# Optimization experiments

Measured on AMD Instinct MI355X. Metric: run time of the kernel, lower is better.

Reference implementation:

```python
import jax, jax.numpy as jnp
import numpy as np

B, S, D = 4, 2048, 1024  # batch, seq_len, isize; FFN hidden = isize, gate dim = 2*isize


def setup_inputs() -> dict:
    key = jax.random.key(0)
    ks = jax.random.split(key, 6)
    sc = lambda n: 1.0 / np.sqrt(n)
    return {
        "iQ": jax.random.normal(ks[0], (B, S, D), jnp.float32),
        "iV": jax.random.normal(ks[1], (B, S, D), jnp.float32),
        "W1": jax.random.normal(ks[2], (D, D), jnp.float32) * sc(D),
        "b1": jnp.zeros((D,), jnp.float32),
        "W2": jax.random.normal(ks[3], (D, D), jnp.float32) * sc(D),
        "b2": jnp.zeros((D,), jnp.float32),
        "Wg": jax.random.normal(ks[4], (2 * D, 2 * D), jnp.float32) * sc(2 * D),
        "bg": jnp.zeros((2 * D,), jnp.float32),
    }


def reference(iQ, iV, W1, b1, W2, b2, Wg, bg):
    seql = iV.shape[1]
    # AAN cumulative-average matrix: row i has 1/(i+1) in cols 0..i (lower triangular)
    inv = 1.0 / jnp.arange(1, seql + 1, dtype=iV.dtype)  # [S]
    attn = jnp.tril(jnp.broadcast_to(inv[:, None], (seql, seql)))  # [S, S]
    avg = jnp.einsum('st,btd->bsd', attn, iV)  # [B, S, D]
    # PositionwiseFF with norm_input=False, dropout=0: Linear -> ReLU -> Linear
    h = jax.nn.relu(avg @ W1 + b1)
    ffn = h @ W2 + b2  # [B, S, D]
    # sigmoid gate over concat(iQ, ffn)
    g = jax.nn.sigmoid(jnp.concatenate([iQ, ffn], axis=-1) @ Wg + bg)  # [B, S, 2D]
    d = ffn.shape[-1]
    igate = g[..., :d]
    fgate = g[..., d:]
    return igate * iQ + fgate * ffn
```

## Files before the change

### kernel.cpp

```cpp
#include <hip/hip_runtime.h>
#include <hip/hip_bf16.h>
#include <cstdint>

typedef unsigned short u16;
typedef unsigned int   u32;

typedef __attribute__((ext_vector_type(8))) short short8;
typedef __attribute__((ext_vector_type(4))) float f32x4;

__device__ __forceinline__ float b2f(u16 v) { return __uint_as_float(((u32)v) << 16); }
__device__ __forceinline__ u16 f2b(float f) {
    u32 u = __float_as_uint(f);
    u += 0x7FFFu + ((u >> 16) & 1u);
    return (u16)(u >> 16);
}

#define G2L16(gp, lp) __builtin_amdgcn_global_load_lds(                       \
    (const __attribute__((address_space(1))) void*)(gp),                      \
    (__attribute__((address_space(3))) void*)(lp), 16, 0, 0)

__device__ __forceinline__ void transpose_body(const float* __restrict__ in,
                                               u16* __restrict__ out,
                                               int R, int C, int lb, int tilesX,
                                               float (*tile)[33]) {
    const int bx = (lb % tilesX) * 32;
    const int by = (lb / tilesX) * 32;
    const int tx = threadIdx.x & 31, ty = threadIdx.x >> 5;
    #pragma unroll
    for (int i = 0; i < 32; i += 8)
        tile[ty + i][tx] = in[(size_t)(by + ty + i) * C + (bx + tx)];
    __syncthreads();
    #pragma unroll
    for (int i = 0; i < 32; i += 8)
        out[(size_t)(bx + ty + i) * R + (by + tx)] = f2b(tile[tx][ty + i]);
}

__global__ void prologue_kernel(const float* __restrict__ W1, u16* __restrict__ W1t,
                                const float* __restrict__ W2, u16* __restrict__ W2t,
                                const float* __restrict__ Wg, u16* __restrict__ Wgt,
                                const float* __restrict__ iQ, u16* __restrict__ iQb,
                                const float* __restrict__ iV, float* __restrict__ csum) {
    __shared__ float tile[32][33];
    const int bid = blockIdx.x;
    const int tid = threadIdx.x;
    if (bid < 1024) {
        transpose_body(W1, W1t, 1024, 1024, bid, 32, tile);
    } else if (bid < 2048) {
        transpose_body(W2, W2t, 1024, 1024, bid - 1024, 32, tile);
    } else if (bid < 6144) {
        transpose_body(Wg, Wgt, 2048, 2048, bid - 2048, 64, tile);
    } else if (bid < 14336) {
        const size_t i = ((size_t)(bid - 6144) * 256 + tid) * 4;
        const float4 v = *(const float4*)(iQ + i);
        ushort4 o;
        o.x = f2b(v.x); o.y = f2b(v.y); o.z = f2b(v.z); o.w = f2b(v.w);
        *(ushort4*)(iQb + i) = o;
    } else {
        const int idx = bid - 14336;
        const int b = idx >> 6, c = idx & 63;
        const int d = tid * 4;
        const float* src = iV + ((size_t)(b * 2048 + c * 32)) * 1024 + d;
        float4 s = {0.f, 0.f, 0.f, 0.f};
        #pragma unroll 8
        for (int i = 0; i < 32; ++i) {
            const float4 v = *(const float4*)(src + (size_t)i * 1024);
            s.x += v.x; s.y += v.y; s.z += v.z; s.w += v.w;
        }
        *(float4*)(csum + ((size_t)(b * 64 + c)) * 1024 + d) = s;
    }
}

__global__ void scan_kernel(const float* __restrict__ iV, const float* __restrict__ csum,
                            u16* __restrict__ avg) {
    const int c = blockIdx.x & 63, b = blockIdx.x >> 6;
    const int d = threadIdx.x * 4;
    const float* cs = csum + (size_t)b * 64 * 1024 + d;
    float4 a0 = {0,0,0,0}, a1 = {0,0,0,0}, a2 = {0,0,0,0}, a3 = {0,0,0,0};
    int cc = 0;
    for (; cc + 4 <= c; cc += 4) {
        const float4 v0 = *(const float4*)(cs + (size_t)(cc + 0) * 1024);
        const float4 v1 = *(const float4*)(cs + (size_t)(cc + 1) * 1024);
        const float4 v2 = *(const float4*)(cs + (size_t)(cc + 2) * 1024);
        const float4 v3 = *(const float4*)(cs + (size_t)(cc + 3) * 1024);
        a0.x += v0.x; a0.y += v0.y; a0.z += v0.z; a0.w += v0.w;
        a1.x += v1.x; a1.y += v1.y; a1.z += v1.z; a1.w += v1.w;
        a2.x += v2.x; a2.y += v2.y; a2.z += v2.z; a2.w += v2.w;
        a3.x += v3.x; a3.y += v3.y; a3.z += v3.z; a3.w += v3.w;
    }
    for (; cc < c; ++cc) {
        const float4 v = *(const float4*)(cs + (size_t)cc * 1024);
        a0.x += v.x; a0.y += v.y; a0.z += v.z; a0.w += v.w;
    }
    float4 acc;
    acc.x = (a0.x + a1.x) + (a2.x + a3.x);
    acc.y = (a0.y + a1.y) + (a2.y + a3.y);
    acc.z = (a0.z + a1.z) + (a2.z + a3.z);
    acc.w = (a0.w + a1.w) + (a2.w + a3.w);

    const size_t off = ((size_t)(b * 2048 + c * 32)) * 1024 + d;
    const float* src = iV + off;
    u16*         dst = avg + off;
    const int s0 = c * 32;
    #pragma unroll 4
    for (int i = 0; i < 32; ++i) {
        const float4 v = *(const float4*)(src + (size_t)i * 1024);
        acc.x += v.x; acc.y += v.y; acc.z += v.z; acc.w += v.w;
        const float inv = 1.0f / (float)(s0 + i + 1);
        ushort4 o;
        o.x = f2b(acc.x * inv); o.y = f2b(acc.y * inv);
        o.z = f2b(acc.z * inv); o.w = f2b(acc.w * inv);
        *(ushort4*)(dst + (size_t)i * 1024) = o;
    }
}

template <int EPI>
__global__ __launch_bounds__(256, 2)
void gemm_kernel(const u16* __restrict__ A, const u16* __restrict__ Bt,
                 const float* __restrict__ bias, u16* __restrict__ C,
                 int M, int N, int K) {
    __shared__ u16 As[128 * 64];
    __shared__ u16 Bs[128 * 64];

    const int tid  = threadIdx.x;
    const int m0   = blockIdx.x * 128;
    const int n0   = blockIdx.y * 128;
    const int wave = tid >> 6, lane = tid & 63;
    const int wm   = (wave & 1) << 6;
    const int wn   = (wave >> 1) << 6;
    const int quad = lane >> 4, l16 = lane & 15;

    f32x4 acc[4][4];
    #pragma unroll
    for (int i = 0; i < 4; ++i)
        #pragma unroll
        for (int j = 0; j < 4; ++j) acc[i][j] = (f32x4){0.f, 0.f, 0.f, 0.f};

    int oo[4], rr[4], qq[4];
    #pragma unroll
    for (int j = 0; j < 4; ++j) {
        oo[j] = tid * 16 + j * 4096;
        rr[j] = oo[j] >> 7;
        qq[j] = ((oo[j] >> 4) & 7) ^ (rr[j] & 7);
    }

    const int ktiles = K >> 6;
    for (int kt = 0; kt < ktiles; ++kt) {
        const int kb = kt << 6;
        #pragma unroll
        for (int j = 0; j < 4; ++j) {
            G2L16((const char*)A  + ((size_t)(m0 + rr[j]) * K + kb) * 2 + qq[j] * 16,
                  (char*)As + oo[j]);
            G2L16((const char*)Bt + ((size_t)(n0 + rr[j]) * K + kb) * 2 + qq[j] * 16,
                  (char*)Bs + oo[j]);
        }
        __syncthreads();

        #pragma unroll
        for (int h = 0; h < 2; ++h) {
            short8 af[4], bf[4];
            #pragma unroll
            for (int mi = 0; mi < 4; ++mi) {
                const int R = wm + mi * 16 + l16;
                af[mi] = *(const short8*)(As + R * 64 + ((((h << 2) | quad) ^ (R & 7)) << 3));
            }
            #pragma unroll
            for (int ni = 0; ni < 4; ++ni) {
                const int R = wn + ni * 16 + l16;
                bf[ni] = *(const short8*)(Bs + R * 64 + ((((h << 2) | quad) ^ (R & 7)) << 3));
            }
            #pragma unroll
            for (int mi = 0; mi < 4; ++mi)
                #pragma unroll
                for (int ni = 0; ni < 4; ++ni)
                    acc[mi][ni] = __builtin_amdgcn_mfma_f32_16x16x32_bf16(
                        af[mi], bf[ni], acc[mi][ni], 0, 0, 0);
        }
        __syncthreads();
    }

    #pragma unroll
    for (int ni = 0; ni < 4; ++ni) {
        const int col = n0 + wn + ni * 16 + l16;
        const float bv = bias[col];
        #pragma unroll
        for (int mi = 0; mi < 4; ++mi) {
            const int row0 = m0 + wm + mi * 16 + quad * 4;
            #pragma unroll
            for (int r = 0; r < 4; ++r) {
                float v = acc[mi][ni][r] + bv;
                if (EPI == 0) v = fmaxf(v, 0.f);
                C[(size_t)(row0 + r) * N + col] = f2b(v);
            }
        }
    }
}

__global__ __launch_bounds__(256, 2)
void gemm_gate_kernel(const u16* __restrict__ iQb, const u16* __restrict__ ffn,
                      const u16* __restrict__ Wgt, const float* __restrict__ bg,
                      const float* __restrict__ iQ, float* __restrict__ out,
                      int M, int D2 ) {
    __shared__ u16 As [128 * 64];
    __shared__ u16 Bs0[128 * 64];
    __shared__ u16 Bs1[128 * 64];

    const int tid  = threadIdx.x;
    const int m0   = blockIdx.x * 128;
    const int n0   = blockIdx.y * 128;
    const int wave = tid >> 6, lane = tid & 63;
    const int wm   = (wave & 1) << 6;
    const int wn   = (wave >> 1) << 6;
    const int quad = lane >> 4, l16 = lane & 15;
    const int D = D2 >> 1;

    f32x4 acc[2][4][4];
    #pragma unroll
    for (int p = 0; p < 2; ++p)
        #pragma unroll
        for (int i = 0; i < 4; ++i)
            #pragma unroll
            for (int j = 0; j < 4; ++j) acc[p][i][j] = (f32x4){0.f, 0.f, 0.f, 0.f};

    int oo[4], rr[4], qq[4];
    #pragma unroll
    for (int j = 0; j < 4; ++j) {
        oo[j] = tid * 16 + j * 4096;
        rr[j] = oo[j] >> 7;
        qq[j] = ((oo[j] >> 4) & 7) ^ (rr[j] & 7);
    }

    const int ktiles = D2 >> 6;
    for (int kt = 0; kt < ktiles; ++kt) {
        const int kb = kt << 6;
        const char* Ab = (const char*)((kb < D) ? (iQb + kb) : (ffn + (kb - D)));
        const char* B0 = (const char*)(Wgt + (size_t)n0 * D2 + kb);
        const char* B1 = (const char*)(Wgt + (size_t)(n0 + D) * D2 + kb);
        #pragma unroll
        for (int j = 0; j < 4; ++j) {
            G2L16(Ab + (size_t)(m0 + rr[j]) * D * 2 + qq[j] * 16, (char*)As  + oo[j]);
            G2L16(B0 + (size_t)rr[j] * D2 * 2 + qq[j] * 16,       (char*)Bs0 + oo[j]);
            G2L16(B1 + (size_t)rr[j] * D2 * 2 + qq[j] * 16,       (char*)Bs1 + oo[j]);
        }
        __syncthreads();

        #pragma unroll
        for (int h = 0; h < 2; ++h) {
            short8 af[4], bf0[4], bf1[4];
            #pragma unroll
            for (int mi = 0; mi < 4; ++mi) {
                const int R = wm + mi * 16 + l16;
                af[mi] = *(const short8*)(As + R * 64 + ((((h << 2) | quad) ^ (R & 7)) << 3));
            }
            #pragma unroll
            for (int ni = 0; ni < 4; ++ni) {
                const int R = wn + ni * 16 + l16;
                const int so = R * 64 + ((((h << 2) | quad) ^ (R & 7)) << 3);
                bf0[ni] = *(const short8*)(Bs0 + so);
                bf1[ni] = *(const short8*)(Bs1 + so);
            }
            #pragma unroll
            for (int mi = 0; mi < 4; ++mi)
                #pragma unroll
                for (int ni = 0; ni < 4; ++ni) {
                    acc[0][mi][ni] = __builtin_amdgcn_mfma_f32_16x16x32_bf16(
                        af[mi], bf0[ni], acc[0][mi][ni], 0, 0, 0);
                    acc[1][mi][ni] = __builtin_amdgcn_mfma_f32_16x16x32_bf16(
                        af[mi], bf1[ni], acc[1][mi][ni], 0, 0, 0);
                }
        }
        __syncthreads();
    }

    #pragma unroll
    for (int ni = 0; ni < 4; ++ni) {
        const int col = n0 + wn + ni * 16 + l16;
        const float bgi = bg[col];
        const float bgf = bg[col + D];
        #pragma unroll
        for (int mi = 0; mi < 4; ++mi) {
            const int row0 = m0 + wm + mi * 16 + quad * 4;
            #pragma unroll
            for (int r = 0; r < 4; ++r) {
                const size_t idx = (size_t)(row0 + r) * D + col;
                const float gi = 1.0f / (1.0f + __expf(-(acc[0][mi][ni][r] + bgi)));
                const float gf = 1.0f / (1.0f + __expf(-(acc[1][mi][ni][r] + bgf)));
                out[idx] = gi * iQ[idx] + gf * b2f(ffn[idx]);
            }
        }
    }
}

extern "C" void kernel_launch(void* const* d_in, const int* in_sizes, int n_in,
                              void* d_out, int out_size, void* d_ws, size_t ws_size,
                              hipStream_t stream) {
    const int B = 4, S = 2048, D = 1024, D2 = 2048;
    const int M = B * S;

    const float* iQ = (const float*)d_in[0];
    const float* iV = (const float*)d_in[1];
    const float* W1 = (const float*)d_in[2];
    const float* b1 = (const float*)d_in[3];
    const float* W2 = (const float*)d_in[4];
    const float* b2 = (const float*)d_in[5];
    const float* Wg = (const float*)d_in[6];
    const float* bg = (const float*)d_in[7];
    float* out = (float*)d_out;

    u16*   regA = (u16*)d_ws;
    u16*   regB = regA + (size_t)M * D;
    u16*   iQb  = regB + (size_t)M * D;
    u16*   W1t  = iQb  + (size_t)M * D;
    u16*   W2t  = W1t  + (size_t)D * D;
    u16*   Wgt  = W2t  + (size_t)D * D;
    float* csum = (float*)(Wgt + (size_t)D2 * D2);

    u16* avg = regA;
    u16* ffn = regA;
    u16* h   = regB;

    prologue_kernel<<<14592, 256, 0, stream>>>(W1, W1t, W2, W2t, Wg, Wgt,
                                               iQ, iQb, iV, csum);
    scan_kernel<<<B * 64, 256, 0, stream>>>(iV, csum, avg);
    gemm_kernel<0><<<dim3(M / 128, D / 128), 256, 0, stream>>>(avg, W1t, b1, h, M, D, D);
    gemm_kernel<1><<<dim3(M / 128, D / 128), 256, 0, stream>>>(h, W2t, b2, ffn, M, D, D);
    gemm_gate_kernel<<<dim3(M / 128, D / 128), 256, 0, stream>>>(
        iQb, ffn, Wgt, bg, iQ, out, M, D2);
}
```

Measured before the change: 266.5 us.

## Replace GEMM kernels with double-buffered 256x128-tile pipelined MFMA kernel

Merges the three GEMM kernels into one templated kernel. It uses 512-thread blocks, 256x128 output tiles and double-buffered LDS staging driven by async global-to-LDS loads, so the next k-slice loads while MFMAs run on the current one. Explicit vmcnt waits, raw barriers and s_setprio replace the per-iteration __syncthreads pattern. The grid shrinks to 256 blocks, one per CU. This cuts the number of tiles and the load-stall bubbles, but the larger LDS footprint (up to 128KB in gate mode) limits occupancy.

```diff
diff --git a/kernel.cpp b/kernel.cpp
--- a/kernel.cpp
+++ b/kernel.cpp
@@ -113,178 +113,166 @@
     }
 }
 
-template <int EPI>
-__global__ __launch_bounds__(256, 2)
-void gemm_kernel(const u16* __restrict__ A, const u16* __restrict__ Bt,
-                 const float* __restrict__ bias, u16* __restrict__ C,
-                 int M, int N, int K) {
-    __shared__ u16 As[128 * 64];
-    __shared__ u16 Bs[128 * 64];
-
-    const int tid  = threadIdx.x;
-    const int m0   = blockIdx.x * 128;
-    const int n0   = blockIdx.y * 128;
-    const int wave = tid >> 6, lane = tid & 63;
-    const int wm   = (wave & 1) << 6;
-    const int wn   = (wave >> 1) << 6;
-    const int quad = lane >> 4, l16 = lane & 15;
-
-    f32x4 acc[4][4];
-    #pragma unroll
-    for (int i = 0; i < 4; ++i)
-        #pragma unroll
-        for (int j = 0; j < 4; ++j) acc[i][j] = (f32x4){0.f, 0.f, 0.f, 0.f};
-
-    int oo[4], rr[4], qq[4];
+template <int MODE>
+__global__ __launch_bounds__(512, 2)
+void gemm_pipe_kernel(const u16* __restrict__ A, const u16* __restrict__ A2,
+                      const u16* __restrict__ Bt, const float* __restrict__ bias,
+                      u16* __restrict__ Cb, const float* __restrict__ iQ,
+                      float* __restrict__ out) {
+    constexpr int NT  = (MODE == 2) ? 32 : 16;
+    constexpr int KBB = ((MODE == 2) ? 2048 : 1024) * 2;
+    constexpr int VPT = (MODE == 2) ? 8 : 6;
+
+    __shared__ u16 As[2][256 * 64];
+    __shared__ u16 Bs[2][(MODE == 2 ? 2 : 1) * 128 * 64];
+
+    const int tid   = threadIdx.x;
+    const int m0    = (blockIdx.x >> 3) * 256;
+    const int n0    = (blockIdx.x & 7) * 128;
+    const int wave  = tid >> 6, lane = tid & 63;
+    const int wm128 = (wave & 1) << 7;
+    const int wn32  = (wave >> 1) << 5;
+    const int quad  = lane >> 4, l16 = lane & 15;
+
+    u32 oA[4], gA[4];
     #pragma unroll
     for (int j = 0; j < 4; ++j) {
-        oo[j] = tid * 16 + j * 4096;
-        rr[j] = oo[j] >> 7;
-        qq[j] = ((oo[j] >> 4) & 7) ^ (rr[j] & 7);
-    }
-
-    const int ktiles = K >> 6;
-    for (int kt = 0; kt < ktiles; ++kt) {
-        const int kb = kt << 6;
-        #pragma unroll
-        for (int j = 0; j < 4; ++j) {
-            G2L16((const char*)A  + ((size_t)(m0 + rr[j]) * K + kb) * 2 + qq[j] * 16,
-                  (char*)As + oo[j]);
-            G2L16((const char*)Bt + ((size_t)(n0 + rr[j]) * K + kb) * 2 + qq[j] * 16,
-                  (char*)Bs + oo[j]);
-        }
-        __syncthreads();
-
+        const u32 o = tid * 16 + j * 8192;
+        const u32 r = o >> 7;
+        const u32 q = ((o >> 4) & 7) ^ (r & 7);
+        oA[j] = o;
+        gA[j] = (u32)(m0 + r) * 2048 + q * 16;
+    }
+    u32 oB[2], gB0[2], gB1[2];
+    #pragma unroll
+    for (int j = 0; j < 2; ++j) {
+        const u32 o = tid * 16 + j * 8192;
+        const u32 r = o >> 7;
+        const u32 q = ((o >> 4) & 7) ^ (r & 7);
+        oB[j] = o;
+        gB0[j] = (u32)(n0 + r) * KBB + q * 16;
+        if (MODE == 2) gB1[j] = (u32)(n0 + 1024 + r) * KBB + q * 16;
+    }
+
+    f32x4 acc0[8][2];
+    f32x4 acc1[(MODE == 2) ? 8 : 1][2];
+    #pragma unroll
+    for (int mi = 0; mi < 8; ++mi)
+        #pragma unroll
+        for (int ni = 0; ni < 2; ++ni) {
+            acc0[mi][ni] = (f32x4){0.f, 0.f, 0.f, 0.f};
+            if constexpr (MODE == 2) acc1[mi][ni] = (f32x4){0.f, 0.f, 0.f, 0.f};
+        }
+
+    auto stage = [&](int b, int t) {
+        const int kb2 = t << 7;
+        const char* Ab;
+        if constexpr (MODE == 2)
+            Ab = (t < 16) ? ((const char*)A + kb2) : ((const char*)A2 + (kb2 - 2048));
+        else
+            Ab = (const char*)A + kb2;
+        #pragma unroll
+        for (int j = 0; j < 4; ++j)
+            G2L16(Ab + gA[j], (char*)&As[b][0] + oA[j]);
+        #pragma unroll
+        for (int j = 0; j < 2; ++j)
+            G2L16((const char*)Bt + kb2 + gB0[j], (char*)&Bs[b][0] + oB[j]);
+        if constexpr (MODE == 2) {
+            #pragma unroll
+            for (int j = 0; j < 2; ++j)
+                G2L16((const char*)Bt + kb2 + gB1[j], (char*)&Bs[b][128 * 64] + oB[j]);
+        }
+    };
+
+    auto compute = [&](int b) {
+        const u16* Asb = &As[b][0];
+        const u16* B0b = &Bs[b][0];
+        const u16* B1b = &Bs[b][(MODE == 2 ? 128 * 64 : 0)];
         #pragma unroll
         for (int h = 0; h < 2; ++h) {
-            short8 af[4], bf[4];
-            #pragma unroll
-            for (int mi = 0; mi < 4; ++mi) {
-                const int R = wm + mi * 16 + l16;
-                af[mi] = *(const short8*)(As + R * 64 + ((((h << 2) | quad) ^ (R & 7)) << 3));
+            const int h4 = h << 2;
+            short8 af[8], b0f[2], b1f[2];
+            #pragma unroll
+            for (int mi = 0; mi < 8; ++mi) {
+                const int R = wm128 + mi * 16 + l16;
+                af[mi] = *(const short8*)(Asb + R * 64 + (((h4 | quad) ^ (R & 7)) << 3));
             }
             #pragma unroll
-            for (int ni = 0; ni < 4; ++ni) {
-                const int R = wn + ni * 16 + l16;
-                bf[ni] = *(const short8*)(Bs + R * 64 + ((((h << 2) | quad) ^ (R & 7)) << 3));
+            for (int ni = 0; ni < 2; ++ni) {
+                const int R = wn32 + ni * 16 + l16;
+                const int so = R * 64 + (((h4 | quad) ^ (R & 7)) << 3);
+                b0f[ni] = *(const short8*)(B0b + so);
+                if constexpr (MODE == 2) b1f[ni] = *(const short8*)(B1b + so);
             }
-            #pragma unroll
-            for (int mi = 0; mi < 4; ++mi)
+            __builtin_amdgcn_s_setprio(1);
+            #pragma unroll
+            for (int mi = 0; mi < 8; ++mi)
                 #pragma unroll
-                for (int ni = 0; ni < 4; ++ni)
-                    acc[mi][ni] = __builtin_amdgcn_mfma_f32_16x16x32_bf16(
-                        af[mi], bf[ni], acc[mi][ni], 0, 0, 0);
-        }
-        __syncthreads();
-    }
-
-    #pragma unroll
-    for (int ni = 0; ni < 4; ++ni) {
-        const int col = n0 + wn + ni * 16 + l16;
-        const float bv = bias[col];
-        #pragma unroll
-        for (int mi = 0; mi < 4; ++mi) {
-            const int row0 = m0 + wm + mi * 16 + quad * 4;
-            #pragma unroll
-            for (int r = 0; r < 4; ++r) {
-                float v = acc[mi][ni][r] + bv;
-                if (EPI == 0) v = fmaxf(v, 0.f);
-                C[(size_t)(row0 + r) * N + col] = f2b(v);
+                for (int ni = 0; ni < 2; ++ni) {
+                    acc0[mi][ni] = __builtin_amdgcn_mfma_f32_16x16x32_bf16(
+                        af[mi], b0f[ni], acc0[mi][ni], 0, 0, 0);
+                    if constexpr (MODE == 2)
+                        acc1[mi][ni] = __builtin_amdgcn_mfma_f32_16x16x32_bf16(
+                            af[mi], b1f[ni], acc1[mi][ni], 0, 0, 0);
+                }
+            __builtin_amdgcn_s_setprio(0);
+        }
+    };
+
+    stage(0, 0);
+    stage(1, 1);
+    asm volatile("s_waitcnt vmcnt(%0)" :: "i"(VPT) : "memory");
+    __builtin_amdgcn_s_barrier();
+    __builtin_amdgcn_sched_barrier(0);
+
+    for (int t = 0; t < NT; ++t) {
+        const int cur = t & 1;
+        compute(cur);
+        __builtin_amdgcn_sched_barrier(0);
+        __builtin_amdgcn_s_barrier();
+        __builtin_amdgcn_sched_barrier(0);
+        if (t + 2 < NT) {
+            stage(cur, t + 2);
+            asm volatile("s_waitcnt vmcnt(%0)" :: "i"(VPT) : "memory");
+        } else if (t + 2 == NT) {
+            asm volatile("s_waitcnt vmcnt(0)" ::: "memory");
+        }
+        __builtin_amdgcn_s_barrier();
+        __builtin_amdgcn_sched_barrier(0);
+    }
+
+    if constexpr (MODE == 2) {
+        #pragma unroll
+        for (int ni = 0; ni < 2; ++ni) {
+            const int col = n0 + wn32 + ni * 16 + l16;
+            const float bgi = bias[col];
+            const float bgf = bias[col + 1024];
+            #pragma unroll
+            for (int mi = 0; mi < 8; ++mi) {
+                const int row0 = m0 + wm128 + mi * 16 + (quad << 2);
+                #pragma unroll
+                for (int r = 0; r < 4; ++r) {
+                    const size_t idx = (size_t)(row0 + r) * 1024 + col;
+                    const float gi = 1.0f / (1.0f + __expf(-(acc0[mi][ni][r] + bgi)));
+                    const float gf = 1.0f / (1.0f + __expf(-(acc1[mi][ni][r] + bgf)));
+                    out[idx] = gi * iQ[idx] + gf * b2f(A2[idx]);
+                }
             }
         }
-    }
-}
-
-__global__ __launch_bounds__(256, 2)
-void gemm_gate_kernel(const u16* __restrict__ iQb, const u16* __restrict__ ffn,
-                      const u16* __restrict__ Wgt, const float* __restrict__ bg,
-                      const float* __restrict__ iQ, float* __restrict__ out,
-                      int M, int D2 ) {
-    __shared__ u16 As [128 * 64];
-    __shared__ u16 Bs0[128 * 64];
-    __shared__ u16 Bs1[128 * 64];
-
-    const int tid  = threadIdx.x;
-    const int m0   = blockIdx.x * 128;
-    const int n0   = blockIdx.y * 128;
-    const int wave = tid >> 6, lane = tid & 63;
-    const int wm   = (wave & 1) << 6;
-    const int wn   = (wave >> 1) << 6;
-    const int quad = lane >> 4, l16 = lane & 15;
-    const int D = D2 >> 1;
-
-    f32x4 acc[2][4][4];
-    #pragma unroll
-    for (int p = 0; p < 2; ++p)
-        #pragma unroll
-        for (int i = 0; i < 4; ++i)
-            #pragma unroll
-            for (int j = 0; j < 4; ++j) acc[p][i][j] = (f32x4){0.f, 0.f, 0.f, 0.f};
-
-    int oo[4], rr[4], qq[4];
-    #pragma unroll
-    for (int j = 0; j < 4; ++j) {
-        oo[j] = tid * 16 + j * 4096;
-        rr[j] = oo[j] >> 7;
-        qq[j] = ((oo[j] >> 4) & 7) ^ (rr[j] & 7);
-    }
-
-    const int ktiles = D2 >> 6;
-    for (int kt = 0; kt < ktiles; ++kt) {
-        const int kb = kt << 6;
-        const char* Ab = (const char*)((kb < D) ? (iQb + kb) : (ffn + (kb - D)));
-        const char* B0 = (const char*)(Wgt + (size_t)n0 * D2 + kb);
-        const char* B1 = (const char*)(Wgt + (size_t)(n0 + D) * D2 + kb);
-        #pragma unroll
-        for (int j = 0; j < 4; ++j) {
-            G2L16(Ab + (size_t)(m0 + rr[j]) * D * 2 + qq[j] * 16, (char*)As  + oo[j]);
-            G2L16(B0 + (size_t)rr[j] * D2 * 2 + qq[j] * 16,       (char*)Bs0 + oo[j]);
-            G2L16(B1 + (size_t)rr[j] * D2 * 2 + qq[j] * 16,       (char*)Bs1 + oo[j]);
-        }
-        __syncthreads();
-
-        #pragma unroll
-        for (int h = 0; h < 2; ++h) {
-            short8 af[4], bf0[4], bf1[4];
-            #pragma unroll
-            for (int mi = 0; mi < 4; ++mi) {
-                const int R = wm + mi * 16 + l16;
-                af[mi] = *(const short8*)(As + R * 64 + ((((h << 2) | quad) ^ (R & 7)) << 3));
-            }
-            #pragma unroll
-            for (int ni = 0; ni < 4; ++ni) {
-                const int R = wn + ni * 16 + l16;
-                const int so = R * 64 + ((((h << 2) | quad) ^ (R & 7)) << 3);
-                bf0[ni] = *(const short8*)(Bs0 + so);
-                bf1[ni] = *(const short8*)(Bs1 + so);
-            }
-            #pragma unroll
-            for (int mi = 0; mi < 4; ++mi)
+    } else {
+        #pragma unroll
+        for (int ni = 0; ni < 2; ++ni) {
+            const int col = n0 + wn32 + ni * 16 + l16;
+            const float bv = bias[col];
+            #pragma unroll
+            for (int mi = 0; mi < 8; ++mi) {
+                const int row0 = m0 + wm128 + mi * 16 + (quad << 2);
                 #pragma unroll
-                for (int ni = 0; ni < 4; ++ni) {
-                    acc[0][mi][ni] = __builtin_amdgcn_mfma_f32_16x16x32_bf16(
-                        af[mi], bf0[ni], acc[0][mi][ni], 0, 0, 0);
-                    acc[1][mi][ni] = __builtin_amdgcn_mfma_f32_16x16x32_bf16(
-                        af[mi], bf1[ni], acc[1][mi][ni], 0, 0, 0);
+                for (int r = 0; r < 4; ++r) {
+                    float v = acc0[mi][ni][r] + bv;
+                    if (MODE == 0) v = fmaxf(v, 0.f);
+                    Cb[(size_t)(row0 + r) * 1024 + col] = f2b(v);
                 }
-        }
-        __syncthreads();
-    }
-
-    #pragma unroll
-    for (int ni = 0; ni < 4; ++ni) {
-        const int col = n0 + wn + ni * 16 + l16;
-        const float bgi = bg[col];
-        const float bgf = bg[col + D];
-        #pragma unroll
-        for (int mi = 0; mi < 4; ++mi) {
-            const int row0 = m0 + wm + mi * 16 + quad * 4;
-            #pragma unroll
-            for (int r = 0; r < 4; ++r) {
-                const size_t idx = (size_t)(row0 + r) * D + col;
-                const float gi = 1.0f / (1.0f + __expf(-(acc[0][mi][ni][r] + bgi)));
-                const float gf = 1.0f / (1.0f + __expf(-(acc[1][mi][ni][r] + bgf)));
-                out[idx] = gi * iQ[idx] + gf * b2f(ffn[idx]);
             }
         }
     }
@@ -321,8 +309,7 @@
     prologue_kernel<<<14592, 256, 0, stream>>>(W1, W1t, W2, W2t, Wg, Wgt,
                                                iQ, iQb, iV, csum);
     scan_kernel<<<B * 64, 256, 0, stream>>>(iV, csum, avg);
-    gemm_kernel<0><<<dim3(M / 128, D / 128), 256, 0, stream>>>(avg, W1t, b1, h, M, D, D);
-    gemm_kernel<1><<<dim3(M / 128, D / 128), 256, 0, stream>>>(h, W2t, b2, ffn, M, D, D);
-    gemm_gate_kernel<<<dim3(M / 128, D / 128), 256, 0, stream>>>(
-        iQb, ffn, Wgt, bg, iQ, out, M, D2);
-}
+    gemm_pipe_kernel<0><<<256, 512, 0, stream>>>(avg, nullptr, W1t, b1, h, nullptr, nullptr);
+    gemm_pipe_kernel<1><<<256, 512, 0, stream>>>(h, nullptr, W2t, b2, ffn, nullptr, nullptr);
+    gemm_pipe_kernel<2><<<256, 512, 0, stream>>>(iQb, ffn, Wgt, bg, nullptr, iQ, out);
+}
```

Result: slower. 305.0 us (+14.4%).

## Rewrite gate GEMM as 8-wave double-buffered pipelined kernel with larger M tile

Applied to the files above, without the earlier changes.

Replaces the gate GEMM with an 8-wave, 512-thread kernel using 256x128 (x2 gate halves) tiles, double-buffered LDS and a hand-scheduled phase sequence. Global-to-LDS loads for upcoming k-tiles are interleaved with MFMA phases, using explicit vmcnt waits, barriers and setprio. The aim is to hide load latency and halve the number of workgroups, which improves B reuse. LDS use grows to 128KB per block, and the hardcoded dimensions and complex scheduling add correctness risk.

```diff
diff --git a/kernel.cpp b/kernel.cpp
--- a/kernel.cpp
+++ b/kernel.cpp
@@ -195,98 +195,159 @@
     }
 }
 
-__global__ __launch_bounds__(256, 2)
-void gemm_gate_kernel(const u16* __restrict__ iQb, const u16* __restrict__ ffn,
-                      const u16* __restrict__ Wgt, const float* __restrict__ bg,
-                      const float* __restrict__ iQ, float* __restrict__ out,
-                      int M, int D2 ) {
-    __shared__ u16 As [128 * 64];
-    __shared__ u16 Bs0[128 * 64];
-    __shared__ u16 Bs1[128 * 64];
+#define VM4  asm volatile("s_waitcnt vmcnt(4)" ::: "memory")
+#define VM0  asm volatile("s_waitcnt vmcnt(0)" ::: "memory")
+#define NOVM ((void)0)
+
+#define SA(BUF, MH, T) do {                                                     \
+    const char* b_ = ((T) < 16) ? ((const char*)iQb + (size_t)(T) * 128)        \
+                                : ((const char*)ffn + (size_t)((T) - 16) * 128); \
+    G2L16(b_ + gA[MH][0], (char*)&As[BUF][MH][0] + lo[0]);                      \
+    G2L16(b_ + gA[MH][1], (char*)&As[BUF][MH][0] + lo[1]);                      \
+  } while (0)
+
+#define SB(BUF, GG, T) do {                                                     \
+    const char* b_ = (const char*)Wgt + (size_t)(T) * 128;                      \
+    G2L16(b_ + gB[GG][0], (char*)&Bs[BUF][GG][0] + lo[0]);                      \
+    G2L16(b_ + gB[GG][1], (char*)&Bs[BUF][GG][0] + lo[1]);                      \
+  } while (0)
+
+#define PHASE(BUF, MH, G, STAGES, VMW) do {                                     \
+    short8 af[4][2], bf[2][2];                                                  \
+    {                                                                           \
+      const char* Ab_ = (const char*)&As[BUF][MH][0];                           \
+      const char* Bb_ = (const char*)&Bs[BUF][G][0];                            \
+      _Pragma("unroll")                                                         \
+      for (int mi = 0; mi < 4; ++mi) {                                          \
+        af[mi][0] = *(const short8*)(Ab_ + aF[mi][0]);                          \
+        af[mi][1] = *(const short8*)(Ab_ + aF[mi][1]);                          \
+      }                                                                         \
+      bf[0][0] = *(const short8*)(Bb_ + bF[0][0]);                              \
+      bf[0][1] = *(const short8*)(Bb_ + bF[0][1]);                              \
+      bf[1][0] = *(const short8*)(Bb_ + bF[1][0]);                              \
+      bf[1][1] = *(const short8*)(Bb_ + bF[1][1]);                              \
+    }                                                                           \
+    STAGES                                                                      \
+    __builtin_amdgcn_sched_barrier(0);                                          \
+    __builtin_amdgcn_s_barrier();                                               \
+    asm volatile("s_waitcnt lgkmcnt(0)" ::: "memory");                          \
+    __builtin_amdgcn_sched_barrier(0);                                          \
+    __builtin_amdgcn_s_setprio(1);                                              \
+    _Pragma("unroll")                                                           \
+    for (int mi = 0; mi < 4; ++mi) {                                            \
+      _Pragma("unroll")                                                         \
+      for (int ni = 0; ni < 2; ++ni) {                                          \
+        acc[G][(MH) * 4 + mi][ni] = __builtin_amdgcn_mfma_f32_16x16x32_bf16(    \
+            af[mi][0], bf[ni][0], acc[G][(MH) * 4 + mi][ni], 0, 0, 0);          \
+        acc[G][(MH) * 4 + mi][ni] = __builtin_amdgcn_mfma_f32_16x16x32_bf16(    \
+            af[mi][1], bf[ni][1], acc[G][(MH) * 4 + mi][ni], 0, 0, 0);          \
+      }                                                                         \
+    }                                                                           \
+    __builtin_amdgcn_s_setprio(0);                                              \
+    __builtin_amdgcn_sched_barrier(0);                                          \
+    VMW;                                                                        \
+    __builtin_amdgcn_s_barrier();                                               \
+    __builtin_amdgcn_sched_barrier(0);                                          \
+  } while (0)
+
+__global__ __launch_bounds__(512, 2)
+void gate8_kernel(const u16* __restrict__ iQb, const u16* __restrict__ ffn,
+                  const u16* __restrict__ Wgt, const float* __restrict__ bg,
+                  const float* __restrict__ iQ, float* __restrict__ out) {
+    __shared__ u16 As[2][2][128 * 64];
+    __shared__ u16 Bs[2][2][128 * 64];
 
     const int tid  = threadIdx.x;
-    const int m0   = blockIdx.x * 128;
-    const int n0   = blockIdx.y * 128;
+    const int bid  = blockIdx.x;
+    const int m0   = (bid & 31) * 256;
+    const int n0   = (bid >> 5) * 128;
     const int wave = tid >> 6, lane = tid & 63;
-    const int wm   = (wave & 1) << 6;
-    const int wn   = (wave >> 1) << 6;
+    const int wm   = wave & 1;
+    const int wn   = wave >> 1;
     const int quad = lane >> 4, l16 = lane & 15;
-    const int D = D2 >> 1;
-
-    f32x4 acc[2][4][4];
-    #pragma unroll
-    for (int p = 0; p < 2; ++p)
-        #pragma unroll
-        for (int i = 0; i < 4; ++i)
-            #pragma unroll
-            for (int j = 0; j < 4; ++j) acc[p][i][j] = (f32x4){0.f, 0.f, 0.f, 0.f};
-
-    int oo[4], rr[4], qq[4];
-    #pragma unroll
-    for (int j = 0; j < 4; ++j) {
-        oo[j] = tid * 16 + j * 4096;
-        rr[j] = oo[j] >> 7;
-        qq[j] = ((oo[j] >> 4) & 7) ^ (rr[j] & 7);
-    }
-
-    const int ktiles = D2 >> 6;
-    for (int kt = 0; kt < ktiles; ++kt) {
-        const int kb = kt << 6;
-        const char* Ab = (const char*)((kb < D) ? (iQb + kb) : (ffn + (kb - D)));
-        const char* B0 = (const char*)(Wgt + (size_t)n0 * D2 + kb);
-        const char* B1 = (const char*)(Wgt + (size_t)(n0 + D) * D2 + kb);
-        #pragma unroll
-        for (int j = 0; j < 4; ++j) {
-            G2L16(Ab + (size_t)(m0 + rr[j]) * D * 2 + qq[j] * 16, (char*)As  + oo[j]);
-            G2L16(B0 + (size_t)rr[j] * D2 * 2 + qq[j] * 16,       (char*)Bs0 + oo[j]);
-            G2L16(B1 + (size_t)rr[j] * D2 * 2 + qq[j] * 16,       (char*)Bs1 + oo[j]);
-        }
-        __syncthreads();
-
-        #pragma unroll
-        for (int h = 0; h < 2; ++h) {
-            short8 af[4], bf0[4], bf1[4];
+
+    u32 lo[2], gA[2][2], gB[2][2];
+    #pragma unroll
+    for (int j = 0; j < 2; ++j) {
+        const u32 o = (u32)tid * 16 + (u32)j * 8192;
+        const u32 r = o >> 7;
+        const u32 q = ((o >> 4) & 7) ^ (r & 7);
+        lo[j]    = o;
+        gA[0][j] = (u32)(m0 + r) * 2048 + q * 16;
+        gA[1][j] = (u32)(m0 + 128 + r) * 2048 + q * 16;
+        gB[0][j] = (u32)(n0 + r) * 4096 + q * 16;
+        gB[1][j] = (u32)(n0 + 1024 + r) * 4096 + q * 16;
+    }
+
+    u32 aF[4][2], bF[2][2];
+    #pragma unroll
+    for (int mi = 0; mi < 4; ++mi) {
+        const int R = wm * 64 + mi * 16 + l16;
+        #pragma unroll
+        for (int ks = 0; ks < 2; ++ks)
+            aF[mi][ks] = (u32)R * 128 + (u32)((((ks << 2) | quad) ^ (R & 7)) << 4);
+    }
+    #pragma unroll
+    for (int ni = 0; ni < 2; ++ni) {
+        const int R = wn * 32 + ni * 16 + l16;
+        #pragma unroll
+        for (int ks = 0; ks < 2; ++ks)
+            bF[ni][ks] = (u32)R * 128 + (u32)((((ks << 2) | quad) ^ (R & 7)) << 4);
+    }
+
+    f32x4 acc[2][8][2];
+    #pragma unroll
+    for (int g = 0; g < 2; ++g)
+        #pragma unroll
+        for (int mf = 0; mf < 8; ++mf)
+            #pragma unroll
+            for (int ni = 0; ni < 2; ++ni)
+                acc[g][mf][ni] = (f32x4){0.f, 0.f, 0.f, 0.f};
+
+    SA(0, 0, 0); SA(0, 1, 0); SB(0, 0, 0); SB(0, 1, 0);
+    SA(1, 0, 1); SB(1, 1, 1);
+    VM4;
+    __builtin_amdgcn_s_barrier();
+    __builtin_amdgcn_sched_barrier(0);
+
+    for (int i = 0; i < 15; ++i) {
+        const int t0 = 2 * i, t1 = t0 + 1;
+        PHASE(0, 0, 0, SA(1, 1, t1);     SB(1, 0, t1);     , NOVM);
+        PHASE(0, 0, 1,                                     , NOVM);
+        PHASE(0, 1, 1, SA(0, 0, t0 + 2);                   , NOVM);
+        PHASE(0, 1, 0, SB(0, 1, t0 + 2);                   , VM4);
+        PHASE(1, 0, 0, SB(0, 0, t0 + 2); SA(0, 1, t0 + 2); , NOVM);
+        PHASE(1, 0, 1,                                     , NOVM);
+        PHASE(1, 1, 1, SA(1, 0, t1 + 2);                   , NOVM);
+        PHASE(1, 1, 0, SB(1, 1, t1 + 2);                   , VM4);
+    }
+    PHASE(0, 0, 0, SA(1, 1, 31); SB(1, 0, 31); , NOVM);
+    PHASE(0, 0, 1,                             , NOVM);
+    PHASE(0, 1, 1,                             , NOVM);
+    PHASE(0, 1, 0,                             , VM0);
+    PHASE(1, 0, 0,                             , NOVM);
+    PHASE(1, 0, 1,                             , NOVM);
+    PHASE(1, 1, 1,                             , NOVM);
+    PHASE(1, 1, 0,                             , NOVM);
+
+    #pragma unroll
+    for (int ni = 0; ni < 2; ++ni) {
+        const int col = n0 + wn * 32 + ni * 16 + l16;
+        const float bgi = bg[col];
+        const float bgf = bg[col + 1024];
+        #pragma unroll
+        for (int mh = 0; mh < 2; ++mh)
             #pragma unroll
             for (int mi = 0; mi < 4; ++mi) {
-                const int R = wm + mi * 16 + l16;
-                af[mi] = *(const short8*)(As + R * 64 + ((((h << 2) | quad) ^ (R & 7)) << 3));
+                const int row0 = m0 + mh * 128 + wm * 64 + mi * 16 + quad * 4;
+                #pragma unroll
+                for (int r = 0; r < 4; ++r) {
+                    const size_t idx = (size_t)(row0 + r) * 1024 + col;
+                    const float gi = 1.0f / (1.0f + __expf(-(acc[0][mh * 4 + mi][ni][r] + bgi)));
+                    const float gf = 1.0f / (1.0f + __expf(-(acc[1][mh * 4 + mi][ni][r] + bgf)));
+                    out[idx] = gi * iQ[idx] + gf * b2f(ffn[idx]);
+                }
             }
-            #pragma unroll
-            for (int ni = 0; ni < 4; ++ni) {
-                const int R = wn + ni * 16 + l16;
-                const int so = R * 64 + ((((h << 2) | quad) ^ (R & 7)) << 3);
-                bf0[ni] = *(const short8*)(Bs0 + so);
-                bf1[ni] = *(const short8*)(Bs1 + so);
-            }
-            #pragma unroll
-            for (int mi = 0; mi < 4; ++mi)
-                #pragma unroll
-                for (int ni = 0; ni < 4; ++ni) {
-                    acc[0][mi][ni] = __builtin_amdgcn_mfma_f32_16x16x32_bf16(
-                        af[mi], bf0[ni], acc[0][mi][ni], 0, 0, 0);
-                    acc[1][mi][ni] = __builtin_amdgcn_mfma_f32_16x16x32_bf16(
-                        af[mi], bf1[ni], acc[1][mi][ni], 0, 0, 0);
-                }
-        }
-        __syncthreads();
-    }
-
-    #pragma unroll
-    for (int ni = 0; ni < 4; ++ni) {
-        const int col = n0 + wn + ni * 16 + l16;
-        const float bgi = bg[col];
-        const float bgf = bg[col + D];
-        #pragma unroll
-        for (int mi = 0; mi < 4; ++mi) {
-            const int row0 = m0 + wm + mi * 16 + quad * 4;
-            #pragma unroll
-            for (int r = 0; r < 4; ++r) {
-                const size_t idx = (size_t)(row0 + r) * D + col;
-                const float gi = 1.0f / (1.0f + __expf(-(acc[0][mi][ni][r] + bgi)));
-                const float gf = 1.0f / (1.0f + __expf(-(acc[1][mi][ni][r] + bgf)));
-                out[idx] = gi * iQ[idx] + gf * b2f(ffn[idx]);
-            }
-        }
     }
 }
 
@@ -323,6 +384,5 @@
     scan_kernel<<<B * 64, 256, 0, stream>>>(iV, csum, avg);
     gemm_kernel<0><<<dim3(M / 128, D / 128), 256, 0, stream>>>(avg, W1t, b1, h, M, D, D);
     gemm_kernel<1><<<dim3(M / 128, D / 128), 256, 0, stream>>>(h, W2t, b2, ffn, M, D, D);
-    gemm_gate_kernel<<<dim3(M / 128, D / 128), 256, 0, stream>>>(
-        iQb, ffn, Wgt, bg, iQ, out, M, D2);
-}
+    gate8_kernel<<<256, 512, 0, stream>>>(iQb, ffn, Wgt, bg, iQ, out);
+}
```

Result: slower. 284.4 us (+6.7%).
